# Kernel optimization log

Hardware: AMD Instinct MI355X
Metric: run time of the kernel (lower is better)

## Reference

```python
import jax, jax.numpy as jnp
import numpy as np

N_EMBD = 1024
D_K = 1024
D_V = 1024

def setup_inputs() -> dict:
    key = jax.random.key(0)
    k1, k2, k3, k4 = jax.random.split(key, 4)
    B, T = 4, 2048
    std = N_EMBD ** -0.5
    x = jax.random.normal(k1, (B, T, N_EMBD), dtype=jnp.float32)
    Wq = jax.random.normal(k2, (N_EMBD, D_K), dtype=jnp.float32) * std
    Wk = jax.random.normal(k3, (N_EMBD, D_K), dtype=jnp.float32) * std
    Wv = jax.random.normal(k4, (N_EMBD, D_V), dtype=jnp.float32) * std
    return {"x": x, "Wq": Wq, "Wk": Wk, "Wv": Wv}

def reference(x, Wq, Wk, Wv):
    # x: [B, T, C]
    T = x.shape[1]
    q = x @ Wq  # [B, T, d_k]
    k = x @ Wk  # [B, T, d_k]
    v = x @ Wv  # [B, T, d_v]
    scale = Wk.shape[1] ** -0.5
    wei = jnp.einsum('btd,bsd->bts', q, k) * scale  # [B, T, T]
    causal = jnp.tril(jnp.ones((T, T), dtype=bool))
    wei = jnp.where(causal, wei, -jnp.inf)
    wei = jax.nn.softmax(wei, axis=-1)
    return wei @ v  # [B, T, d_v]
```

## Files before the change

### kernel.cpp

```cpp
#include <hip/hip_runtime.h>
#include <hip/hip_bf16.h>
#include <stdint.h>

using bf16_t = __hip_bfloat16;
typedef __bf16 bf16x8 __attribute__((ext_vector_type(8)));
typedef float f32x4 __attribute__((ext_vector_type(4)));

__device__ __forceinline__ void async_lds16(const void* g, void* l) {
  __builtin_amdgcn_global_load_lds(
      (const __attribute__((address_space(1))) void*)g,
      (__attribute__((address_space(3))) void*)l, 16, 0, 0);
}

__device__ __forceinline__ unsigned short f2bf_u16(float f) {
  __hip_bfloat16 h = __float2bfloat16(f);
  return __builtin_bit_cast(unsigned short, h);
}

__device__ __forceinline__ float bf2f(unsigned short u) {
  __hip_bfloat16 h = __builtin_bit_cast(__hip_bfloat16, u);
  return __bfloat162float(h);
}

__global__ __launch_bounds__(256) void convert_all_kernel(
    const float* __restrict__ x, bf16_t* __restrict__ xb,
    const float* __restrict__ Wq, const float* __restrict__ Wk,
    const float* __restrict__ Wv, bf16_t* __restrict__ wt) {
  __shared__ bf16_t tile[32][33];
  const int bid = blockIdx.x;
  if (bid < 8192) {
    size_t i = ((size_t)bid * 256 + threadIdx.x) * 4;
    float4 v = *(const float4*)(x + i);
    ushort4 o;
    o.x = f2bf_u16(v.x);
    o.y = f2bf_u16(v.y);
    o.z = f2bf_u16(v.z);
    o.w = f2bf_u16(v.w);
    *(ushort4*)(xb + i) = o;
    return;
  }
  const int w = bid - 8192;
  const int z = w >> 10;
  const int bxy = w & 1023;
  const float* W = (z == 0) ? Wq : (z == 1) ? Wk : Wv;
  bf16_t* WT = wt + (size_t)z * 1024 * 1024;
  const int tx = threadIdx.x & 31;
  const int ty = threadIdx.x >> 5;
  const int bx = bxy & 31;
  const int by = bxy >> 5;
  const int k0 = by * 32, n0 = bx * 32;
#pragma unroll
  for (int j = 0; j < 32; j += 8)
    tile[ty + j][tx] = __float2bfloat16(W[(size_t)(k0 + ty + j) * 1024 + n0 + tx]);
  __syncthreads();
#pragma unroll
  for (int j = 0; j < 32; j += 8)
    WT[(size_t)(n0 + ty + j) * 1024 + k0 + tx] = tile[tx][ty + j];
}

template <int OUT_MODE>
__global__ __launch_bounds__(512, 2) void gemm_proj_kernel(
    const bf16_t* __restrict__ A, const bf16_t* __restrict__ BT,
    void* __restrict__ Cv, void* __restrict__ Cv2, void* __restrict__ Cv3,
    int K, int lda, int ldb) {
  int bx = blockIdx.x, by = blockIdx.y;
  {
    const int gx = gridDim.x;
    const int nwg = gx * gridDim.y;
    const int id = by * gx + bx;
    const int cpx = nwg >> 3;
    const int swz = (id & 7) * cpx + (id >> 3);
    by = swz / gx;
    bx = swz % gx;
  }
  const int m0 = by * 128;
  const int n0 = bx * 256;
  const int nkt = K >> 5;

  __shared__ bf16_t lsA[2 * 4096];
  __shared__ bf16_t lsB[2 * 8192];

  const int tid = threadIdx.x;
  const int wid = tid >> 6;
  const int lane = tid & 63;
  const int wm = wid >> 2;
  const int wn = wid & 3;

  const int sr = tid >> 2;
  const int sswz = (tid & 3) ^ ((sr >> 1) & 3);
  const bf16_t* gA = A + (size_t)(m0 + sr) * lda + sswz * 8;
  const bf16_t* gB0 = BT + (size_t)(n0 + sr) * ldb + sswz * 8;
  const bf16_t* gB1 = BT + (size_t)(n0 + 128 + sr) * ldb + sswz * 8;

  const int kslot = (lane >> 4) ^ ((lane >> 1) & 3);
  const int abase = (wm * 64 + (lane & 15)) * 32 + kslot * 8;
  const int bbase = (wn * 64 + (lane & 15)) * 32 + kslot * 8;

  auto stage = [&](int t) {
    const int buf = t & 1;
    bf16_t* dA = lsA + buf * 4096 + wid * 512;
    bf16_t* dB = lsB + buf * 8192 + wid * 512;
    const size_t co = (size_t)t * 32;
    async_lds16(gA + co, dA);
    async_lds16(gB0 + co, dB);
    async_lds16(gB1 + co, dB + 4096);
  };

  f32x4 acc[4][4];
  const f32x4 zero = {0.f, 0.f, 0.f, 0.f};
#pragma unroll
  for (int m = 0; m < 4; ++m)
#pragma unroll
    for (int n = 0; n < 4; ++n) acc[m][n] = zero;

  stage(0);
  asm volatile("s_waitcnt vmcnt(0)" ::: "memory");
  __builtin_amdgcn_s_barrier();

  for (int t = 0; t < nkt; ++t) {
    const bf16_t* bufA = lsA + (t & 1) * 4096;
    const bf16_t* bufB = lsB + (t & 1) * 8192;
    if (t + 1 < nkt) stage(t + 1);

    bf16x8 af[4], bfr[4];
#pragma unroll
    for (int mf = 0; mf < 4; ++mf)
      af[mf] = *(const bf16x8*)(bufA + abase + mf * 512);
#pragma unroll
    for (int nf = 0; nf < 4; ++nf)
      bfr[nf] = *(const bf16x8*)(bufB + bbase + nf * 512);

    __builtin_amdgcn_s_setprio(1);
#pragma unroll
    for (int mf = 0; mf < 4; ++mf)
#pragma unroll
      for (int nf = 0; nf < 4; ++nf)
        acc[mf][nf] = __builtin_amdgcn_mfma_f32_16x16x32_bf16(
            af[mf], bfr[nf], acc[mf][nf], 0, 0, 0);
    __builtin_amdgcn_s_setprio(0);

    if (t + 1 < nkt) {
      asm volatile("s_waitcnt vmcnt(0)" ::: "memory");
    }
    __builtin_amdgcn_s_barrier();
  }

  const int erow = wm * 64 + (lane >> 4) * 4;
  const int ecol = wn * 64 + (lane & 15);
  if (n0 < 2048) {
    bf16_t* C = (bf16_t*)((n0 < 1024) ? Cv : Cv2);
    const int cb0 = n0 & 1023;
#pragma unroll
    for (int m = 0; m < 4; ++m)
#pragma unroll
      for (int n = 0; n < 4; ++n)
#pragma unroll
        for (int j = 0; j < 4; ++j) {
          int r = m0 + erow + m * 16 + j;
          int c = cb0 + ecol + n * 16;
          C[(size_t)r * 1024 + c] = __float2bfloat16(acc[m][n][j]);
        }
  } else {
    bf16_t* C = (bf16_t*)Cv3;
    const int d0 = n0 - 2048;
#pragma unroll
    for (int m = 0; m < 4; ++m)
#pragma unroll
      for (int n = 0; n < 4; ++n)
#pragma unroll
        for (int j = 0; j < 4; ++j) {
          int r = m0 + erow + m * 16 + j;
          int d = d0 + ecol + n * 16;
          int b = r >> 11, tt = r & 2047;
          C[((size_t)b * 1024 + d) * 2048 + tt] = __float2bfloat16(acc[m][n][j]);
        }
  }
}

template <int OUT_MODE, bool CAUSAL_SKIP, bool PAIRED>
__global__ __launch_bounds__(512, 2) void gemm128_kernel(
    const bf16_t* __restrict__ A, const bf16_t* __restrict__ BT,
    void* __restrict__ Cv, int K, int lda, int ldb, int ldc,
    long long aBatch, long long bBatch, long long cBatch) {
  const int bx = blockIdx.x, by = blockIdx.y;
  if (CAUSAL_SKIP && bx > by) return;
  const bf16_t* Ab = A + (size_t)blockIdx.z * aBatch;
  const bf16_t* Bb = BT + (size_t)blockIdx.z * bBatch;

  __shared__ bf16_t lsA[3 * 4096];
  __shared__ bf16_t lsB[3 * 4096];

  const int tid = threadIdx.x;
  const int wid = tid >> 6;
  const int lane = tid & 63;
  const int wm = wid >> 2;
  const int wn = wid & 3;

  const int sr = tid >> 2;
  const int sswz = (tid & 3) ^ ((sr >> 1) & 3);
  const int n0 = bx * 128;
  const bf16_t* gB = Bb + (size_t)(n0 + sr) * ldb + sswz * 8;

  const int kslot = (lane >> 4) ^ ((lane >> 1) & 3);
  const int aRd = (wm * 64 + (lane & 15)) * 32 + kslot * 8;
  const int bRd = (wn * 32 + (lane & 15)) * 32 + kslot * 8;

  const int njobs = PAIRED ? 2 : 1;
  for (int job = 0; job < njobs; ++job) {
    const int byE = (PAIRED && job) ? (15 - by) : by;
    const int m0 = byE * 128;
    int nkt = K >> 5;
    if (PAIRED) {
      int lim = (m0 + 128) >> 5;
      nkt = nkt < lim ? nkt : lim;
    }
    const bf16_t* gA = Ab + (size_t)(m0 + sr) * lda + sswz * 8;

    f32x4 acc[4][2];
    const f32x4 zero = {0.f, 0.f, 0.f, 0.f};
#pragma unroll
    for (int m = 0; m < 4; ++m)
#pragma unroll
      for (int n = 0; n < 2; ++n) acc[m][n] = zero;

    async_lds16(gA, lsA + wid * 512);
    async_lds16(gB, lsB + wid * 512);
    if (nkt > 1) {
      async_lds16(gA + 32, lsA + 4096 + wid * 512);
      async_lds16(gB + 32, lsB + 4096 + wid * 512);
      asm volatile("s_waitcnt vmcnt(2)" ::: "memory");
    } else {
      asm volatile("s_waitcnt vmcnt(0)" ::: "memory");
    }
    __builtin_amdgcn_s_barrier();

    int cb = 0;
    for (int t = 0; t < nkt; ++t) {
      const bf16_t* bufA = lsA + cb * 4096;
      const bf16_t* bufB = lsB + cb * 4096;
      int sb = cb + 2;
      if (sb >= 3) sb -= 3;

      bf16x8 af[4], bfr[2];
#pragma unroll
      for (int mf = 0; mf < 4; ++mf)
        af[mf] = *(const bf16x8*)(bufA + aRd + mf * 512);
      bfr[0] = *(const bf16x8*)(bufB + bRd);
      bfr[1] = *(const bf16x8*)(bufB + bRd + 512);
      if (t + 2 < nkt) {
        async_lds16(gA + (t + 2) * 32, lsA + sb * 4096 + wid * 512);
        async_lds16(gB + (t + 2) * 32, lsB + sb * 4096 + wid * 512);
        asm volatile("s_waitcnt vmcnt(2)" ::: "memory");
      } else if (t + 2 == nkt) {
        asm volatile("s_waitcnt vmcnt(0)" ::: "memory");
      }
      __builtin_amdgcn_s_barrier();
      __builtin_amdgcn_s_setprio(1);
#pragma unroll
      for (int mf = 0; mf < 4; ++mf)
#pragma unroll
        for (int nf = 0; nf < 2; ++nf)
          acc[mf][nf] = __builtin_amdgcn_mfma_f32_16x16x32_bf16(
              af[mf], bfr[nf], acc[mf][nf], 0, 0, 0);
      __builtin_amdgcn_s_setprio(0);
      __builtin_amdgcn_s_barrier();

      cb = cb + 1;
      if (cb >= 3) cb -= 3;
    }

    const int erow = wm * 64 + (lane >> 4) * 4;
    const int ecol = wn * 32 + (lane & 15);
    if (OUT_MODE == 2) {
      float* C = (float*)Cv + (size_t)blockIdx.z * cBatch;
#pragma unroll
      for (int m = 0; m < 4; ++m)
#pragma unroll
        for (int n = 0; n < 2; ++n)
#pragma unroll
          for (int j = 0; j < 4; ++j) {
            int r = m0 + erow + m * 16 + j;
            int c = n0 + ecol + n * 16;
            C[(size_t)r * ldc + c] = acc[m][n][j];
          }
    } else {
      bf16_t* C = (bf16_t*)Cv + (size_t)blockIdx.z * cBatch;
#pragma unroll
      for (int m = 0; m < 4; ++m)
#pragma unroll
        for (int n = 0; n < 2; ++n)
#pragma unroll
          for (int j = 0; j < 4; ++j) {
            int r = m0 + erow + m * 16 + j;
            int c = n0 + ecol + n * 16;
            C[(size_t)r * ldc + c] = __float2bfloat16(acc[m][n][j]);
          }
    }
  }
}

__global__ __launch_bounds__(256) void softmax_causal_kernel(bf16_t* __restrict__ Sb) {
  const int lane = threadIdx.x & 63;
  const int rg = blockIdx.x * 4 + (threadIdx.x >> 6);
  const int b = rg >> 11;
  const int t = rg & 2047;
  bf16_t* srow = Sb + (size_t)b * 8388608 + (size_t)t * 4096;
  const int qmax = t >> 8;

  float v[8][4];
#pragma unroll
  for (int it = 0; it < 8; ++it) {
    if (it <= qmax) {
      ushort4 u = *(const ushort4*)(srow + (it * 64 + lane) * 4);
      v[it][0] = bf2f(u.x);
      v[it][1] = bf2f(u.y);
      v[it][2] = bf2f(u.z);
      v[it][3] = bf2f(u.w);
    } else {
      v[it][0] = v[it][1] = v[it][2] = v[it][3] = 0.f;
    }
  }

  float mx = -3.0e38f;
#pragma unroll
  for (int it = 0; it < 8; ++it) {
    int s0 = (it * 64 + lane) * 4;
    if (s0 + 0 <= t) mx = fmaxf(mx, v[it][0]);
    if (s0 + 1 <= t) mx = fmaxf(mx, v[it][1]);
    if (s0 + 2 <= t) mx = fmaxf(mx, v[it][2]);
    if (s0 + 3 <= t) mx = fmaxf(mx, v[it][3]);
  }
#pragma unroll
  for (int off = 32; off > 0; off >>= 1) mx = fmaxf(mx, __shfl_xor(mx, off, 64));

  const float kMul = 0.03125f * 1.4426950408889634f;
  float p[8][4];
  float sum = 0.f;
#pragma unroll
  for (int it = 0; it < 8; ++it) {
    int s0 = (it * 64 + lane) * 4;
    float e0 = (s0 + 0 <= t) ? exp2f((v[it][0] - mx) * kMul) : 0.f;
    float e1 = (s0 + 1 <= t) ? exp2f((v[it][1] - mx) * kMul) : 0.f;
    float e2 = (s0 + 2 <= t) ? exp2f((v[it][2] - mx) * kMul) : 0.f;
    float e3 = (s0 + 3 <= t) ? exp2f((v[it][3] - mx) * kMul) : 0.f;
    p[it][0] = e0; p[it][1] = e1; p[it][2] = e2; p[it][3] = e3;
    sum += (e0 + e1) + (e2 + e3);
  }
#pragma unroll
  for (int off = 32; off > 0; off >>= 1) sum += __shfl_xor(sum, off, 64);
  const float inv = 1.f / sum;

#pragma unroll
  for (int it = 0; it < 8; ++it) {
    if (it <= qmax) {
      ushort4 o;
      o.x = f2bf_u16(p[it][0] * inv);
      o.y = f2bf_u16(p[it][1] * inv);
      o.z = f2bf_u16(p[it][2] * inv);
      o.w = f2bf_u16(p[it][3] * inv);
      *(ushort4*)(srow + (it * 64 + lane) * 4) = o;
    }
  }
}

extern "C" void kernel_launch(void* const* d_in, const int* in_sizes, int n_in,
                              void* d_out, int out_size, void* d_ws, size_t ws_size,
                              hipStream_t stream) {
  (void)in_sizes; (void)n_in; (void)out_size;
  const float* x = (const float*)d_in[0];
  const float* Wq = (const float*)d_in[1];
  const float* Wk = (const float*)d_in[2];
  const float* Wv = (const float*)d_in[3];
  float* out = (float*)d_out;

  char* ws = (char*)d_ws;
  const size_t NEED = 123731968;
  const bool batched = ws_size >= NEED;

  bf16_t* xb = (bf16_t*)ws;
  bf16_t* Sb;
  bf16_t *WT, *Qb, *Kb, *VT;
  if (batched) {
    Sb = (bf16_t*)ws;
    WT = (bf16_t*)(ws + 67108864);
    Qb = (bf16_t*)(ws + 73400320);
    Kb = (bf16_t*)(ws + 90177536);
    VT = (bf16_t*)(ws + 106954752);
  } else {
    Sb = (bf16_t*)ws;
    WT = (bf16_t*)(ws + 16777216);
    Qb = (bf16_t*)(ws + 16777216 + 6291456);
    Kb = Qb + 8388608;
    VT = Kb + 8388608;
  }

  convert_all_kernel<<<11264, 256, 0, stream>>>(x, xb, Wq, Wk, Wv, WT);

  gemm_proj_kernel<3><<<dim3(12, 64, 1), 512, 0, stream>>>(
      xb, WT, Qb, Kb, VT, 1024, 1024, 1024);

  const int nbat = batched ? 4 : 1;
  for (int pass = 0; pass < (batched ? 1 : 4); ++pass) {
    const size_t qoff = (size_t)pass * 2048 * 1024;
    const bf16_t* Qp = Qb + qoff;
    const bf16_t* Kp = Kb + qoff;
    const bf16_t* Vp = VT + qoff;
    float* op = out + qoff;
    gemm128_kernel<5, true, false><<<dim3(16, 16, nbat), 512, 0, stream>>>(
        Qp, Kp, Sb, 1024, 1024, 1024, 4096,
        batched ? 2097152LL : 0, batched ? 2097152LL : 0,
        batched ? 8388608LL : 0);
    softmax_causal_kernel<<<batched ? 2048 : 512, 256, 0, stream>>>(Sb);
    gemm128_kernel<2, false, true><<<dim3(8, 8, nbat), 512, 0, stream>>>(
        Sb, Vp, op, 2048, 4096, 2048, 1024,
        batched ? 8388608LL : 0, batched ? 2097152LL : 0,
        batched ? 2097152LL : 0);
  }
}
```

Measured before the change: 177.4 us.

## Replace double-buffered projection GEMM with single-buffer 128x128 tile kernel

The QKV projection GEMM moves from a 512-thread, 128x256-tile, double-buffered async-LDS pipeline to a 256-thread, 128x128-tile kernel with one LDS buffer and two barriers per k-step. The grid doubles to 24x64 blocks and LDS per block drops, so more blocks can be resident and occupancy may hide latency instead of software prefetch. The trade-off is that global-to-LDS loads are no longer overlapped with MFMA work inside a block, the setprio hints are gone, and B-tile reuse per block is halved. The epilogue still assumes n0 below 2048 selects Q/K output, which stays consistent with 128-wide tiles.

```diff
diff --git a/kernel.cpp b/kernel.cpp
--- a/kernel.cpp
+++ b/kernel.cpp
@@ -59,7 +59,7 @@
 }
 
 template <int OUT_MODE>
-__global__ __launch_bounds__(512, 2) void gemm_proj_kernel(
+__global__ __launch_bounds__(256) void gemm_m97_kernel(
     const bf16_t* __restrict__ A, const bf16_t* __restrict__ BT,
     void* __restrict__ Cv, void* __restrict__ Cv2, void* __restrict__ Cv3,
     int K, int lda, int ldb) {
@@ -74,37 +74,28 @@
     bx = swz % gx;
   }
   const int m0 = by * 128;
-  const int n0 = bx * 256;
+  const int n0 = bx * 128;
   const int nkt = K >> 5;
 
-  __shared__ bf16_t lsA[2 * 4096];
-  __shared__ bf16_t lsB[2 * 8192];
+  __shared__ bf16_t lsA[4096];
+  __shared__ bf16_t lsB[4096];
 
   const int tid = threadIdx.x;
   const int wid = tid >> 6;
   const int lane = tid & 63;
-  const int wm = wid >> 2;
-  const int wn = wid & 3;
+  const int wm = wid >> 1;
+  const int wn = wid & 1;
 
   const int sr = tid >> 2;
   const int sswz = (tid & 3) ^ ((sr >> 1) & 3);
   const bf16_t* gA = A + (size_t)(m0 + sr) * lda + sswz * 8;
-  const bf16_t* gB0 = BT + (size_t)(n0 + sr) * ldb + sswz * 8;
-  const bf16_t* gB1 = BT + (size_t)(n0 + 128 + sr) * ldb + sswz * 8;
+  const bf16_t* gB = BT + (size_t)(n0 + sr) * ldb + sswz * 8;
+  const size_t gA64 = (size_t)64 * lda;
+  const size_t gB64 = (size_t)64 * ldb;
 
   const int kslot = (lane >> 4) ^ ((lane >> 1) & 3);
-  const int abase = (wm * 64 + (lane & 15)) * 32 + kslot * 8;
-  const int bbase = (wn * 64 + (lane & 15)) * 32 + kslot * 8;
-
-  auto stage = [&](int t) {
-    const int buf = t & 1;
-    bf16_t* dA = lsA + buf * 4096 + wid * 512;
-    bf16_t* dB = lsB + buf * 8192 + wid * 512;
-    const size_t co = (size_t)t * 32;
-    async_lds16(gA + co, dA);
-    async_lds16(gB0 + co, dB);
-    async_lds16(gB1 + co, dB + 4096);
-  };
+  const int aoff = (wm * 64 + (lane & 15)) * 32 + kslot * 8;
+  const int boff = (wn * 64 + (lane & 15)) * 32 + kslot * 8;
 
   f32x4 acc[4][4];
   const f32x4 zero = {0.f, 0.f, 0.f, 0.f};
@@ -113,36 +104,28 @@
 #pragma unroll
     for (int n = 0; n < 4; ++n) acc[m][n] = zero;
 
-  stage(0);
-  asm volatile("s_waitcnt vmcnt(0)" ::: "memory");
-  __builtin_amdgcn_s_barrier();
-
-  for (int t = 0; t < nkt; ++t) {
-    const bf16_t* bufA = lsA + (t & 1) * 4096;
-    const bf16_t* bufB = lsB + (t & 1) * 8192;
-    if (t + 1 < nkt) stage(t + 1);
+  for (int kt = 0; kt < nkt; ++kt) {
+    __syncthreads();
+    const size_t co = (size_t)kt * 32;
+    async_lds16(gA + co, lsA + wid * 512);
+    async_lds16(gA + co + gA64, lsA + 2048 + wid * 512);
+    async_lds16(gB + co, lsB + wid * 512);
+    async_lds16(gB + co + gB64, lsB + 2048 + wid * 512);
+    __syncthreads();
 
     bf16x8 af[4], bfr[4];
 #pragma unroll
     for (int mf = 0; mf < 4; ++mf)
-      af[mf] = *(const bf16x8*)(bufA + abase + mf * 512);
+      af[mf] = *(const bf16x8*)(lsA + aoff + mf * 512);
 #pragma unroll
     for (int nf = 0; nf < 4; ++nf)
-      bfr[nf] = *(const bf16x8*)(bufB + bbase + nf * 512);
-
-    __builtin_amdgcn_s_setprio(1);
+      bfr[nf] = *(const bf16x8*)(lsB + boff + nf * 512);
 #pragma unroll
     for (int mf = 0; mf < 4; ++mf)
 #pragma unroll
       for (int nf = 0; nf < 4; ++nf)
         acc[mf][nf] = __builtin_amdgcn_mfma_f32_16x16x32_bf16(
             af[mf], bfr[nf], acc[mf][nf], 0, 0, 0);
-    __builtin_amdgcn_s_setprio(0);
-
-    if (t + 1 < nkt) {
-      asm volatile("s_waitcnt vmcnt(0)" ::: "memory");
-    }
-    __builtin_amdgcn_s_barrier();
   }
 
   const int erow = wm * 64 + (lane >> 4) * 4;
@@ -396,7 +379,7 @@
 
   convert_all_kernel<<<11264, 256, 0, stream>>>(x, xb, Wq, Wk, Wv, WT);
 
-  gemm_proj_kernel<3><<<dim3(12, 64, 1), 512, 0, stream>>>(
+  gemm_m97_kernel<3><<<dim3(24, 64, 1), 256, 0, stream>>>(
       xb, WT, Qb, Kb, VT, 1024, 1024, 1024);
 
   const int nbat = batched ? 4 : 1;
```

Result: no change. 179.9 us (+1.4%).
